# Optimization experiments

Measured on AMD Instinct MI355X. Metric: run time of the kernel, lower is better.

## Reference

```python
import jax, jax.numpy as jnp
import numpy as np

B, C, T, H, W = 8, 256, 16, 28, 28
RED = 2
CR = C // RED
BN_EPS = 1e-5


def conv1x1(x, w, b):
    # x: [b,c,t,h,w], w: [out,c], b: [out] -> [b,out,t,h,w]
    return jnp.einsum('oc,bcthw->bothw', w, x) + b[None, :, None, None, None]


def setup_inputs() -> dict:
    key = jax.random.key(0)
    ks = jax.random.split(key, 12)
    s_in = 1.0 / np.sqrt(C)
    s_cr = 1.0 / np.sqrt(CR)
    return {
        'x': jax.random.normal(ks[0], (B, C, T, H, W), dtype=jnp.float32),
        'Wq': jax.random.normal(ks[1], (CR, C), dtype=jnp.float32) * s_in,
        'bq': jax.random.normal(ks[2], (CR,), dtype=jnp.float32) * 0.01,
        'Wk': jax.random.normal(ks[3], (CR, C), dtype=jnp.float32) * s_in,
        'bk': jax.random.normal(ks[4], (CR,), dtype=jnp.float32) * 0.01,
        'Wv': jax.random.normal(ks[5], (CR, C), dtype=jnp.float32) * s_in,
        'bv': jax.random.normal(ks[6], (CR,), dtype=jnp.float32) * 0.01,
        'Wr': jax.random.normal(ks[7], (C, CR), dtype=jnp.float32) * s_cr,
        'br': jax.random.normal(ks[8], (C,), dtype=jnp.float32) * 0.01,
        'gamma': 1.0 + 0.1 * jax.random.normal(ks[9], (C,), dtype=jnp.float32),
        'beta': 0.1 * jax.random.normal(ks[10], (C,), dtype=jnp.float32),
        'bn_mean': 0.1 * jax.random.normal(ks[11], (C,), dtype=jnp.float32),
        'bn_var': jnp.ones((C,), dtype=jnp.float32),
    }


def reference(x, Wq, bq, Wk, bk, Wv, bv, Wr, br, gamma, beta, bn_mean, bn_var):
    b, c, t, h, w = x.shape
    cr = c // RED
    hw = h * w
    k_top = hw // 4

    Q = conv1x1(x, Wq, bq).reshape(b * cr, t, hw)
    K = conv1x1(x, Wk, bk).reshape(b * cr, t, hw)
    V = conv1x1(x, Wv, bv).reshape(b * cr, t, hw)

    # top-k (descending, sorted) along spatial dim
    Q_tk, _ = jax.lax.top_k(Q, k_top)  # [b*cr, t, k]
    K_tk, _ = jax.lax.top_k(K, k_top)  # [b*cr, t, k]

    corr = jnp.einsum('ntk,nsk->nts', Q_tk, K_tk)  # [b*cr, t, t]
    attn = jax.nn.softmax(corr, axis=-1)
    y = jnp.einsum('nts,nsp->ntp', attn, V)        # [b*cr, t, hw]
    y = y.reshape(b, cr, t, h, w)

    # reconstruct: 1x1 conv + BatchNorm3d (eval-mode with running stats)
    y = conv1x1(y, Wr, br)
    scale = gamma / jnp.sqrt(bn_var + BN_EPS)
    y = y * scale[None, :, None, None, None] + (beta - bn_mean * scale)[None, :, None, None, None]
    return y + x
```

## Files before the change

### kernel.cpp

```cpp
#include <hip/hip_runtime.h>
#include <hip/hip_bf16.h>
#include <cfloat>

#define B_   8
#define C_   256
#define CR_  128
#define T_   16
#define HW_  784
#define THW_ 12544
#define N_   1024
#define KTOP 196

typedef __attribute__((ext_vector_type(8))) short short8;
typedef __attribute__((ext_vector_type(8))) _Float16 half8;
typedef __attribute__((ext_vector_type(4))) float float4_;

__device__ __forceinline__ unsigned short f2bf(float x) {
    unsigned int u = __float_as_uint(x);
    unsigned int r = u + 0x7fffu + ((u >> 16) & 1u);
    return (unsigned short)(r >> 16);
}
__device__ __forceinline__ float bf2f(unsigned short s) {
    return __uint_as_float(((unsigned int)s) << 16);
}
__device__ __forceinline__ void splith(float v, unsigned short& h, unsigned short& l) {
    _Float16 hh = (_Float16)v;
    _Float16 ll = (_Float16)(v - (float)hh);
    h = __builtin_bit_cast(unsigned short, hh);
    l = __builtin_bit_cast(unsigned short, ll);
}

__global__ __launch_bounds__(256) void prep(
    const float* __restrict__ Wq, const float* __restrict__ Wk,
    const float* __restrict__ Wv, const float* __restrict__ Wr,
    const float* __restrict__ bq, const float* __restrict__ bk,
    const float* __restrict__ bv, const float* __restrict__ br,
    const float* __restrict__ gamma, const float* __restrict__ beta,
    const float* __restrict__ bn_mean, const float* __restrict__ bn_var,
    unsigned short* __restrict__ W16,
    unsigned short* __restrict__ Wrbf, float* __restrict__ bias3,
    float* __restrict__ A1, float* __restrict__ A2)
{
    int idx = blockIdx.x * 256 + threadIdx.x;
    if (idx < 384 * 256) {
        int o = idx >> 8, k = idx & 255;
        int m = o >> 7, r = o & 127;
        const float* W = (m == 0) ? Wq : (m == 1) ? Wk : Wv;
        float v = W[r * 256 + k];
        _Float16 hh = (_Float16)v;
        W16[idx] = __builtin_bit_cast(unsigned short, hh);
    }
    if (idx < 256 * 128) {
        Wrbf[idx] = f2bf(Wr[idx]);
    }
    if (idx < 384) {
        bias3[idx] = (idx < 128) ? bq[idx] : (idx < 256) ? bk[idx - 128] : bv[idx - 256];
    }
    if (idx < 256) {
        float sc = gamma[idx] * rsqrtf(bn_var[idx] + 1e-5f);
        A1[idx] = sc;
        A2[idx] = br[idx] * sc + beta[idx] - bn_mean[idx] * sc;
    }
}

__global__ __launch_bounds__(512, 4) void gemm_qkv_mfma(
    const unsigned short* __restrict__ W16,
    const float* __restrict__ x, const float* __restrict__ bias3,
    float* __restrict__ Qb, float* __restrict__ Kb, float* __restrict__ Vb)
{
    const int tid  = threadIdx.x;
    const int wave = tid >> 6;
    const int lane = tid & 63;
    const int quad = lane >> 4;
    const int l16  = lane & 15;
    const int p0   = blockIdx.x * 64;
    const int b    = blockIdx.y;
    const int mW   = wave * 48;

    __shared__ unsigned short Ald[2][384][36];
    __shared__ unsigned short Bld[2][2][64][40];

    float4_ acc[3][4];
#pragma unroll
    for (int i = 0; i < 3; i++)
#pragma unroll
        for (int j = 0; j < 4; j++) acc[i][j] = (float4_)0.f;

    const float* xb = x + (size_t)b * C_ * THW_;
    const int sp  = lane;
    const int kgB = wave * 4;

    {
#pragma unroll
        for (int it = 0; it < 6; it++) {
            int c = tid + it * 512, row = c >> 3, part = c & 7;
            *(uint2*)&Ald[0][row][part * 4] =
                *(const uint2*)&W16[(size_t)row * 256 + part * 4];
        }
        float f[4];
#pragma unroll
        for (int j = 0; j < 4; j++)
            f[j] = xb[(size_t)(kgB + j) * THW_ + p0 + sp];
#pragma unroll
        for (int j = 0; j < 4; j++) {
            unsigned short hh, ll; splith(f[j], hh, ll);
            Bld[0][0][sp][kgB + j] = hh;
            Bld[0][1][sp][kgB + j] = ll;
        }
    }
    __syncthreads();

#pragma unroll 2
    for (int ks = 0; ks < 8; ks++) {
        const int cur = ks & 1;
        const int k0n = (ks + 1) * 32;

        uint2 au[6];
        float f[4];
        if (ks < 7) {
#pragma unroll
            for (int it = 0; it < 6; it++) {
                int c = tid + it * 512, row = c >> 3, part = c & 7;
                au[it] = *(const uint2*)&W16[(size_t)row * 256 + k0n + part * 4];
            }
#pragma unroll
            for (int j = 0; j < 4; j++)
                f[j] = xb[(size_t)(k0n + kgB + j) * THW_ + p0 + sp];
        }

        short8 Bh[4], Bl[4];
#pragma unroll
        for (int nf = 0; nf < 4; nf++) {
            Bh[nf] = *(const short8*)&Bld[cur][0][nf * 16 + l16][quad * 8];
            Bl[nf] = *(const short8*)&Bld[cur][1][nf * 16 + l16][quad * 8];
        }

#pragma unroll
        for (int mf = 0; mf < 3; mf++) {
            const unsigned short* ap = &Ald[cur][mW + mf * 16 + l16][quad * 8];
            half8 Af;
            *(uint2*)&Af       = *(const uint2*)ap;
            *((uint2*)&Af + 1) = *(const uint2*)(ap + 4);
#pragma unroll
            for (int nf = 0; nf < 4; nf++) {
                acc[mf][nf] = __builtin_amdgcn_mfma_f32_16x16x32_f16(
                    Af, *(const half8*)&Bl[nf], acc[mf][nf], 0, 0, 0);
                acc[mf][nf] = __builtin_amdgcn_mfma_f32_16x16x32_f16(
                    Af, *(const half8*)&Bh[nf], acc[mf][nf], 0, 0, 0);
            }
        }

        if (ks < 7) {
#pragma unroll
            for (int it = 0; it < 6; it++) {
                int c = tid + it * 512, row = c >> 3, part = c & 7;
                *(uint2*)&Ald[cur ^ 1][row][part * 4] = au[it];
            }
#pragma unroll
            for (int j = 0; j < 4; j++) {
                unsigned short hh, ll; splith(f[j], hh, ll);
                Bld[cur ^ 1][0][sp][kgB + j] = hh;
                Bld[cur ^ 1][1][sp][kgB + j] = ll;
            }
        }
        __syncthreads();
    }

#pragma unroll
    for (int mf = 0; mf < 3; mf++) {
#pragma unroll
        for (int r = 0; r < 4; r++) {
            int oo  = mW + mf * 16 + quad * 4 + r;
            int mat = oo >> 7;
            int cr  = oo & 127;
            float bi = bias3[oo];
            float* dst = ((mat == 0) ? Qb : (mat == 1) ? Kb : Vb)
                         + ((size_t)(b * 128 + cr)) * THW_ + p0 + l16;
#pragma unroll
            for (int nf = 0; nf < 4; nf++)
                dst[nf * 16] = acc[mf][nf][r] + bi;
        }
    }
}

__global__ __launch_bounds__(256) void topk_sort_wave(
    const float* __restrict__ Qb, const float* __restrict__ Kb,
    float* __restrict__ Qtk, float* __restrict__ Ktk)
{
    const int wave = threadIdx.x >> 6;
    const int lane = threadIdx.x & 63;
    const int half = lane >> 5;
    const int L    = lane & 31;
    const int gw   = (blockIdx.x * 4 + wave) * 2 + half;
    const int mat  = gw >> 14;
    const int row  = gw & 16383;
    const float* src = ((mat == 0) ? Qb : Kb) + (size_t)row * HW_;
    float* dst       = ((mat == 0) ? Qtk : Ktk) + (size_t)row * KTOP;

    float v[32];
    if (L < 24) {
        const float4* s4 = (const float4*)(src + L * 32);
#pragma unroll
        for (int q = 0; q < 8; q++) {
            float4 t = s4[q];
            v[q * 4 + 0] = t.x; v[q * 4 + 1] = t.y;
            v[q * 4 + 2] = t.z; v[q * 4 + 3] = t.w;
        }
    } else if (L == 24) {
        const float4* s4 = (const float4*)(src + 768);
#pragma unroll
        for (int q = 0; q < 4; q++) {
            float4 t = s4[q];
            v[q * 4 + 0] = t.x; v[q * 4 + 1] = t.y;
            v[q * 4 + 2] = t.z; v[q * 4 + 3] = t.w;
        }
#pragma unroll
        for (int r = 16; r < 32; r++) v[r] = -FLT_MAX;
    } else {
#pragma unroll
        for (int r = 0; r < 32; r++) v[r] = -FLT_MAX;
    }

#pragma unroll
    for (int k = 2; k <= 1024; k <<= 1) {
#pragma unroll
        for (int j = k >> 1; j >= 1; j >>= 1) {
            if (j >= 32) {
                const int jl = j >> 5;
                const bool up      = ((L & (k >> 5)) == 0);
                const bool isLower = ((L & jl) == 0);
                const bool keepMax = (up == isLower);
#pragma unroll
                for (int r = 0; r < 32; r++) {
                    float other = __shfl_xor(v[r], jl, 64);
                    float mx = fmaxf(v[r], other);
                    float mn = fminf(v[r], other);
                    v[r] = keepMax ? mx : mn;
                }
            } else {
#pragma unroll
                for (int r = 0; r < 32; r++) {
                    if ((r & j) == 0) {
                        const int rb = r | j;
                        const bool up = (k >= 32) ? ((L & (k >> 5)) == 0)
                                                  : ((r & k) == 0);
                        float a = v[r], b = v[rb];
                        float hi = fmaxf(a, b), lo = fminf(a, b);
                        v[r]  = up ? hi : lo;
                        v[rb] = up ? lo : hi;
                    }
                }
            }
        }
    }

    if (L < 6) {
        float4* d4 = (float4*)(dst + L * 32);
#pragma unroll
        for (int q = 0; q < 8; q++) {
            float4 t;
            t.x = v[q * 4 + 0]; t.y = v[q * 4 + 1];
            t.z = v[q * 4 + 2]; t.w = v[q * 4 + 3];
            d4[q] = t;
        }
    } else if (L == 6) {
        float4 t;
        t.x = v[0]; t.y = v[1]; t.z = v[2]; t.w = v[3];
        *(float4*)(dst + 192) = t;
    }
}

__global__ __launch_bounds__(256) void corr_softmax(
    const float* __restrict__ Qtk, const float* __restrict__ Ktk,
    float* __restrict__ attn)
{
    const int n = blockIdx.x;
    __shared__ float qs[T_ * KTOP];
    __shared__ float ks[T_ * KTOP];
    __shared__ float cm[T_][T_ + 1];
    __shared__ float mx[T_], sm[T_];
    const int tid = threadIdx.x;

    for (int i = tid; i < T_ * KTOP; i += 256) {
        qs[i] = Qtk[(size_t)n * T_ * KTOP + i];
        ks[i] = Ktk[(size_t)n * T_ * KTOP + i];
    }
    __syncthreads();

    const int t = tid >> 4, sidx = tid & 15;
    const float* qr = &qs[t * KTOP];
    const float* kr = &ks[sidx * KTOP];
    float c = 0.f;
#pragma unroll 4
    for (int i = 0; i < KTOP; i++) c += qr[i] * kr[i];
    cm[t][sidx] = c;
    __syncthreads();

    if (tid < T_) {
        float m = cm[tid][0];
        for (int i = 1; i < T_; i++) m = fmaxf(m, cm[tid][i]);
        mx[tid] = m;
    }
    __syncthreads();
    float e = expf(c - mx[t]);
    cm[t][sidx] = e;
    __syncthreads();
    if (tid < T_) {
        float ssum = 0.f;
        for (int i = 0; i < T_; i++) ssum += cm[tid][i];
        sm[tid] = ssum;
    }
    __syncthreads();
    attn[(size_t)n * 256 + tid] = e / sm[t];
}

__global__ __launch_bounds__(256) void apply_attn_T(
    const float* __restrict__ attn, const float* __restrict__ V,
    unsigned short* __restrict__ yT)
{
    const int pc = blockIdx.x;
    const int b  = blockIdx.y;
    const int p0 = pc * 16;
    const int tid = threadIdx.x;
    const int crl = tid & 15;
    const int g   = tid >> 4;

    __shared__ float at[16][257];
    __shared__ float vt[16][260];

    for (int chunk = 0; chunk < 8; chunk++) {
        const int crbase = chunk * 16;
        for (int i = tid; i < 16 * 256; i += 256) {
            int cr = i >> 8, ts = i & 255;
            at[cr][ts] = attn[((size_t)(b * 128 + crbase + cr)) * 256 + ts];
        }
        for (int i = tid; i < 16 * 256; i += 256) {
            int cr = i >> 8, s = (i >> 4) & 15, p = i & 15;
            vt[cr][s * 16 + p] =
                V[((size_t)(b * 128 + crbase + cr)) * THW_ + s * HW_ + p0 + p];
        }
        __syncthreads();

        const int cr = crbase + crl;
        float a[16];
#pragma unroll
        for (int s = 0; s < 16; s++) a[s] = at[crl][g * 16 + s];
        float sum[16];
#pragma unroll
        for (int p = 0; p < 16; p++) sum[p] = 0.f;
#pragma unroll
        for (int s = 0; s < 16; s++) {
            const float as = a[s];
#pragma unroll
            for (int p4 = 0; p4 < 4; p4++) {
                float4 vv = *(const float4*)&vt[crl][s * 16 + p4 * 4];
                sum[p4 * 4 + 0] += as * vv.x;
                sum[p4 * 4 + 1] += as * vv.y;
                sum[p4 * 4 + 2] += as * vv.z;
                sum[p4 * 4 + 3] += as * vv.w;
            }
        }
        const size_t obase = (size_t)b * THW_ + (size_t)g * HW_ + p0;
#pragma unroll
        for (int p = 0; p < 16; p++)
            yT[(obase + p) * 128 + cr] = f2bf(sum[p]);
        __syncthreads();
    }
}

__global__ __launch_bounds__(256, 3) void gemm_recon_mfma(
    const unsigned short* __restrict__ Wrbf, const unsigned short* __restrict__ yT,
    const float* __restrict__ A1, const float* __restrict__ A2,
    const float* __restrict__ x, float* __restrict__ out)
{
    const int tid  = threadIdx.x;
    const int wave = tid >> 6;
    const int lane = tid & 63;
    const int quad = lane >> 4;
    const int l16  = lane & 15;
    const int p0   = blockIdx.x * 64;
    const int coB  = blockIdx.y * 128;
    const int b    = blockIdx.z;
    const int mW   = wave * 32;

    __shared__ unsigned short Wld[128][136];
    __shared__ unsigned short Yld[64][136];

#pragma unroll
    for (int it = 0; it < 8; it++) {
        int c = tid + it * 256, row = c >> 4, part = c & 15;
        *(uint4*)&Wld[row][part * 8] =
            *(const uint4*)&Wrbf[(size_t)(coB + row) * 128 + part * 8];
    }
    const unsigned short* yTb = yT + ((size_t)b * THW_ + p0) * 128;
#pragma unroll
    for (int it = 0; it < 4; it++) {
        int c = tid + it * 256, row = c >> 4, part = c & 15;
        *(uint4*)&Yld[row][part * 8] =
            *(const uint4*)&yTb[(size_t)row * 128 + part * 8];
    }
    __syncthreads();

    float4_ acc[2][4];
#pragma unroll
    for (int i = 0; i < 2; i++)
#pragma unroll
        for (int j = 0; j < 4; j++) acc[i][j] = (float4_)0.f;

#pragma unroll
    for (int k0 = 0; k0 < 128; k0 += 32) {
        short8 Bf[4];
#pragma unroll
        for (int nf = 0; nf < 4; nf++)
            Bf[nf] = *(const short8*)&Yld[nf * 16 + l16][k0 + quad * 8];
#pragma unroll
        for (int mf = 0; mf < 2; mf++) {
            short8 Af = *(const short8*)&Wld[mW + mf * 16 + l16][k0 + quad * 8];
#pragma unroll
            for (int nf = 0; nf < 4; nf++)
                acc[mf][nf] = __builtin_amdgcn_mfma_f32_16x16x32_bf16(Af, Bf[nf], acc[mf][nf], 0, 0, 0);
        }
    }

#pragma unroll
    for (int mf = 0; mf < 2; mf++) {
#pragma unroll
        for (int r = 0; r < 4; r++) {
            int co = coB + mW + mf * 16 + quad * 4 + r;
            float sc = A1[co], sh = A2[co];
            size_t base = ((size_t)b * 256 + co) * THW_ + p0 + l16;
#pragma unroll
            for (int nf = 0; nf < 4; nf++) {
                float xv = x[base + nf * 16];
                out[base + nf * 16] = acc[mf][nf][r] * sc + sh + xv;
            }
        }
    }
}

extern "C" void kernel_launch(void* const* d_in, const int* in_sizes, int n_in,
                              void* d_out, int out_size, void* d_ws, size_t ws_size,
                              hipStream_t stream)
{
    const float* x      = (const float*)d_in[0];
    const float* Wq     = (const float*)d_in[1];
    const float* bq     = (const float*)d_in[2];
    const float* Wk     = (const float*)d_in[3];
    const float* bk     = (const float*)d_in[4];
    const float* Wv     = (const float*)d_in[5];
    const float* bv     = (const float*)d_in[6];
    const float* Wr     = (const float*)d_in[7];
    const float* br     = (const float*)d_in[8];
    const float* gamma  = (const float*)d_in[9];
    const float* beta   = (const float*)d_in[10];
    const float* bn_mean= (const float*)d_in[11];
    const float* bn_var = (const float*)d_in[12];
    float* out = (float*)d_out;

    float* Qb = out;
    float* Kb = out + (size_t)N_ * THW_;

    char* ws = (char*)d_ws;
    float* Vb            = (float*)ws;                       ws += (size_t)N_ * THW_ * 4;
    unsigned short* yT   = (unsigned short*)ws;              ws += (size_t)N_ * THW_ * 2;
    float* Qtk           = (float*)ws;                       ws += (size_t)N_ * T_ * KTOP * 4;
    float* Ktk           = (float*)ws;                       ws += (size_t)N_ * T_ * KTOP * 4;
    float* attn          = (float*)ws;                       ws += (size_t)N_ * T_ * T_ * 4;
    unsigned short* W16  = (unsigned short*)ws;              ws += 384 * 256 * 2;
    unsigned short* Wrbf = (unsigned short*)ws;              ws += 256 * 128 * 2;
    float* bias3         = (float*)ws;                       ws += 384 * 4;
    float* A1            = (float*)ws;                       ws += 256 * 4;
    float* A2            = (float*)ws;                       ws += 256 * 4;

    prep<<<dim3(384), 256, 0, stream>>>(Wq, Wk, Wv, Wr, bq, bk, bv, br,
                                        gamma, beta, bn_mean, bn_var,
                                        W16, Wrbf, bias3, A1, A2);
    gemm_qkv_mfma<<<dim3(196, 8), 512, 0, stream>>>(W16, x, bias3, Qb, Kb, Vb);
    topk_sort_wave<<<dim3(4096), 256, 0, stream>>>(Qb, Kb, Qtk, Ktk);
    corr_softmax<<<dim3(1024), 256, 0, stream>>>(Qtk, Ktk, attn);
    apply_attn_T<<<dim3(49, 8), 256, 0, stream>>>(attn, Vb, yT);
    gemm_recon_mfma<<<dim3(196, 2, 8), 256, 0, stream>>>(Wrbf, yT, A1, A2, x, out);
}
```

Before: 497.0 us.

## Replace full bitonic sort with 256-sort plus bitonic top-k merges

Instead of fully sorting all 1024 candidates per row, each 256-element block is sorted descending. Blocks are then reduced pairwise with max-merges of reversed partners followed by bitonic cleanup, keeping only the top 256. This removes the later stages of the 1024-wide sort, cutting shuffle and compare work in the top-k step. Correctness depends on the lane/register xor masks pairing reversed elements properly.

```diff
diff --git a/kernel.cpp b/kernel.cpp
--- a/kernel.cpp
+++ b/kernel.cpp
@@ -222,12 +222,12 @@
     }
 
 #pragma unroll
-    for (int k = 2; k <= 1024; k <<= 1) {
+    for (int k = 2; k <= 256; k <<= 1) {
 #pragma unroll
         for (int j = k >> 1; j >= 1; j >>= 1) {
             if (j >= 32) {
                 const int jl = j >> 5;
-                const bool up      = ((L & (k >> 5)) == 0);
+                const bool up = (k == 256) ? true : ((L & (k >> 5)) == 0);
                 const bool isLower = ((L & jl) == 0);
                 const bool keepMax = (up == isLower);
 #pragma unroll
@@ -242,12 +242,49 @@
                 for (int r = 0; r < 32; r++) {
                     if ((r & j) == 0) {
                         const int rb = r | j;
-                        const bool up = (k >= 32) ? ((L & (k >> 5)) == 0)
+                        const bool up = (k == 256) ? true
+                                      : (k >= 32) ? ((L & (k >> 5)) == 0)
                                                   : ((r & k) == 0);
                         float a = v[r], b = v[rb];
                         float hi = fmaxf(a, b), lo = fminf(a, b);
                         v[r]  = up ? hi : lo;
                         v[rb] = up ? lo : hi;
+                    }
+                }
+            }
+        }
+    }
+
+#pragma unroll
+    for (int m = 0; m < 2; m++) {
+        const int mask = m ? 23 : 15;
+#pragma unroll
+        for (int r = 0; r < 16; r++) {
+            float a = __shfl_xor(v[31 - r], mask, 64);
+            float b = __shfl_xor(v[r],      mask, 64);
+            v[r]      = fmaxf(v[r],      a);
+            v[31 - r] = fmaxf(v[31 - r], b);
+        }
+#pragma unroll
+        for (int j = 128; j >= 1; j >>= 1) {
+            if (j >= 32) {
+                const int jl = j >> 5;
+                const bool keepMax = ((L & jl) == 0);
+#pragma unroll
+                for (int r = 0; r < 32; r++) {
+                    float other = __shfl_xor(v[r], jl, 64);
+                    float mx = fmaxf(v[r], other);
+                    float mn = fminf(v[r], other);
+                    v[r] = keepMax ? mx : mn;
+                }
+            } else {
+#pragma unroll
+                for (int r = 0; r < 32; r++) {
+                    if ((r & j) == 0) {
+                        const int rb = r | j;
+                        float a = v[r], b = v[rb];
+                        v[r]  = fmaxf(a, b);
+                        v[rb] = fminf(a, b);
                     }
                 }
             }
```

Result: faster. 483.5 us (-2.7%).
